# Kernel tuning notes

Hardware: AMD Instinct MI355X
Metric: run time of the kernel (lower is better)

Reference implementation:

```python
import jax, jax.numpy as jnp
import numpy as np

B, T, N, D = 2, 256, 128, 512
H = 8
D_INNER, D_STATE, D_CONV, DT_RANK = 2 * D, 16, 4, D // 16  # mamba defaults
EPS = 1e-5


def setup_inputs() -> dict:
    key = jax.random.key(0)
    ks = iter(jax.random.split(key, 32))
    g = lambda shape, s=0.02: jax.random.normal(next(ks), shape, dtype=jnp.float32) * s
    return {
        "x": jax.random.normal(next(ks), (B, T, N, D), dtype=jnp.float32),
        "mha_in_w": g((3 * D, D)), "mha_in_b": jnp.zeros((3 * D,), jnp.float32),
        "mha_out_w": g((D, D)), "mha_out_b": jnp.zeros((D,), jnp.float32),
        "n1_w": jnp.ones((D,), jnp.float32),
        "n2_w": jnp.ones((D,), jnp.float32),
        "n3_w": jnp.ones((D,), jnp.float32),
        "m_in_w": g((2 * D_INNER, D)),
        "m_conv_w": g((D_INNER, 1, D_CONV), 0.1), "m_conv_b": jnp.zeros((D_INNER,), jnp.float32),
        "m_xproj_w": g((DT_RANK + 2 * D_STATE, D_INNER)),
        "m_dt_w": g((D_INNER, DT_RANK)), "m_dt_b": jnp.full((D_INNER,), -4.6, jnp.float32),
        "m_A_log": jnp.tile(jnp.log(jnp.arange(1, D_STATE + 1, dtype=jnp.float32)), (D_INNER, 1)),
        "m_D": jnp.ones((D_INNER,), jnp.float32),
        "m_out_w": g((D, D_INNER)),
        "mlp_w1": g((2 * D, D)), "mlp_b1": jnp.zeros((2 * D,), jnp.float32),
        "mlp_w2": g((D, 2 * D)), "mlp_b2": jnp.zeros((D,), jnp.float32),
    }


def rmsnorm(x, w):
    return x * jax.lax.rsqrt(jnp.mean(x * x, axis=-1, keepdims=True) + EPS) * w


def mha(x, in_w, in_b, out_w, out_b):
    # x: (Bt, N, D); torch nn.MultiheadAttention with batch_first=True
    Bt, n, d = x.shape
    dh = d // H
    qkv = x @ in_w.T + in_b
    q, k, v = jnp.split(qkv, 3, axis=-1)
    q = q.reshape(Bt, n, H, dh)
    k = k.reshape(Bt, n, H, dh)
    v = v.reshape(Bt, n, H, dh)
    att = jax.nn.softmax(jnp.einsum('bnhd,bmhd->bhnm', q, k) / jnp.sqrt(jnp.float32(dh)), axis=-1)
    o = jnp.einsum('bhnm,bmhd->bnhd', att, v).reshape(Bt, n, d)
    return o @ out_w.T + out_b


def mamba(x, in_w, conv_w, conv_b, xproj_w, dt_w, dt_b, A_log, Dp, out_w):
    # x: (Bm, L, D)  -- standard mamba_ssm Mamba block (expand=2, d_state=16, d_conv=4)
    Bm, L, _ = x.shape
    xz = x @ in_w.T                      # (Bm, L, 2*d_inner)
    xm, z = jnp.split(xz, 2, axis=-1)
    # causal depthwise conv1d along time
    xc = jnp.pad(xm.transpose(0, 2, 1), ((0, 0), (0, 0), (D_CONV - 1, 0)))
    xc = jax.lax.conv_general_dilated(xc, conv_w, (1,), 'VALID',
                                      dimension_numbers=('NCH', 'OIH', 'NCH'),
                                      feature_group_count=D_INNER)
    xm = jax.nn.silu(xc.transpose(0, 2, 1) + conv_b)   # (Bm, L, d_inner)
    x_dbl = xm @ xproj_w.T
    dt, Bs, Cs = jnp.split(x_dbl, [DT_RANK, DT_RANK + D_STATE], axis=-1)
    dt = jax.nn.softplus(dt @ dt_w.T + dt_b)           # (Bm, L, d_inner)
    A = -jnp.exp(A_log)                                # (d_inner, d_state)

    def step(h, inp):
        dt_t, B_t, C_t, u_t = inp                      # (Bm,d_in),(Bm,ds),(Bm,ds),(Bm,d_in)
        dA = jnp.exp(dt_t[:, :, None] * A)             # (Bm, d_inner, d_state)
        h = dA * h + (dt_t * u_t)[:, :, None] * B_t[:, None, :]
        y = jnp.einsum('bds,bs->bd', h, C_t)
        return h, y

    h0 = jnp.zeros((Bm, D_INNER, D_STATE), x.dtype)
    inputs = (dt.transpose(1, 0, 2), Bs.transpose(1, 0, 2),
              Cs.transpose(1, 0, 2), xm.transpose(1, 0, 2))
    _, ys = jax.lax.scan(step, h0, inputs)
    y = ys.transpose(1, 0, 2) + xm * Dp
    y = y * jax.nn.silu(z)
    return y @ out_w.T


def reference(x, mha_in_w, mha_in_b, mha_out_w, mha_out_b, n1_w, n2_w, n3_w,
              m_in_w, m_conv_w, m_conv_b, m_xproj_w, m_dt_w, m_dt_b, m_A_log, m_D, m_out_w,
              mlp_w1, mlp_b1, mlp_w2, mlp_b2):
    Bx, Tx, Nx, Dx = x.shape
    # spatial attention over regions
    xs = x.reshape(Bx * Tx, Nx, Dx)
    xs = rmsnorm(xs + mha(xs, mha_in_w, mha_in_b, mha_out_w, mha_out_b), n1_w)
    # temporal mamba over time
    xt = xs.reshape(Bx, Tx, Nx, Dx).transpose(0, 2, 1, 3).reshape(Bx * Nx, Tx, Dx)
    xt = rmsnorm(xt + mamba(xt, m_in_w, m_conv_w, m_conv_b, m_xproj_w,
                            m_dt_w, m_dt_b, m_A_log, m_D, m_out_w), n2_w)
    # MLP (1 hidden layer, width 2*D, ReLU)
    x3 = xt.reshape(Bx, Nx, Tx, Dx).transpose(0, 2, 1, 3)
    h = jax.nn.relu(x3 @ mlp_w1.T + mlp_b1) @ mlp_w2.T + mlp_b2
    return rmsnorm(x3 + h, n3_w)
```

## Files before the change

### kernel.cpp

```cpp
#include <hip/hip_runtime.h>

typedef unsigned short u16;
typedef unsigned int u32;
typedef __attribute__((ext_vector_type(8))) short short8;
typedef __attribute__((ext_vector_type(4))) float f32x4;

__device__ __forceinline__ float bf2f(u16 u){ union{u32 i; float f;} v; v.i=((u32)u)<<16; return v.f; }
__device__ __forceinline__ u16 f2bf(float f){ union{float f; u32 i;} v; v.f=f; u32 r=v.i+0x7FFFu+((v.i>>16)&1u); return (u16)(r>>16); }

__device__ __forceinline__ void glds16(const u16* g, u16* lds){
  __builtin_amdgcn_global_load_lds((const __attribute__((address_space(1))) u32*)g,
                                   (__attribute__((address_space(3))) u32*)lds, 16, 0, 0);
}

__global__ __launch_bounds__(256) void cvt_kernel(const float* __restrict__ src, u16* __restrict__ dst, int n4){
  int i = blockIdx.x*256 + threadIdx.x;
  if (i >= n4) return;
  float4 v = ((const float4*)src)[i];
  union { u16 o[4]; uint2 q; } t;
  t.o[0]=f2bf(v.x); t.o[1]=f2bf(v.y); t.o[2]=f2bf(v.z); t.o[3]=f2bf(v.w);
  ((uint2*)dst)[i] = t.q;
}

template<int BM, int BN, int EPI>
__global__ __launch_bounds__(256, 2) void gemm_bt_kernel(
    const u16* __restrict__ A, int lda,
    const u16* __restrict__ B,
    const float* __restrict__ bias,
    u16* __restrict__ C, int ldc,
    int N, int K)
{
  constexpr int RM = BM/32, RN = BN/32;
  constexpr int AI = BM/64, BI = BN/64;
  const int tid = threadIdx.x;
  const int wave = tid>>6, lane = tid&63;
  const int wm = wave>>1, wn = wave&1;
  const int lm = lane&15, quad = lane>>4;
  const int bm0 = blockIdx.x*BM, bn0 = blockIdx.y*BN;
  __shared__ __align__(16) u16 As[BM*32];
  __shared__ __align__(16) u16 Bs[BN*32];
  f32x4 acc[RM][RN] = {};
  const int vr = tid>>2, vc = (tid&3)<<3;
  for (int k0=0; k0<K; k0+=32){
    __syncthreads();
    #pragma unroll
    for (int i=0;i<AI;i++)
      glds16(A + (size_t)(bm0 + i*64 + vr)*lda + k0 + vc, &As[(i*256 + wave*64)*8]);
    #pragma unroll
    for (int i=0;i<BI;i++)
      glds16(B + (size_t)(bn0 + i*64 + vr)*K + k0 + vc, &Bs[(i*256 + wave*64)*8]);
    __syncthreads();
    short8 af[RM], bfr[RN];
    #pragma unroll
    for (int i=0;i<RM;i++) af[i] = *(const short8*)(&As[(wm*(BM/2)+i*16+lm)*32 + quad*8]);
    #pragma unroll
    for (int j=0;j<RN;j++) bfr[j] = *(const short8*)(&Bs[(wn*(BN/2)+j*16+lm)*32 + quad*8]);
    #pragma unroll
    for (int i=0;i<RM;i++)
      #pragma unroll
      for (int j=0;j<RN;j++)
        acc[i][j] = __builtin_amdgcn_mfma_f32_16x16x32_bf16(af[i], bfr[j], acc[i][j], 0,0,0);
  }
  #pragma unroll
  for (int j=0;j<RN;j++){
    int col = bn0 + wn*(BN/2) + j*16 + lm;
    float bv = 0.f;
    if (EPI >= 1) bv = bias[col];
    #pragma unroll
    for (int i=0;i<RM;i++){
      int r0 = bm0 + wm*(BM/2) + i*16 + quad*4;
      #pragma unroll
      for (int r=0;r<4;r++){
        float v = acc[i][j][r] + bv;
        if (EPI == 2) v = fmaxf(v, 0.f);
        if (EPI == 3) v = (v > 20.f) ? v : log1pf(__expf(v));
        C[(size_t)(r0+r)*ldc + col] = f2bf(v);
      }
    }
  }
}

__global__ __launch_bounds__(256, 2) void attn_kernel(const u16* __restrict__ qkv, u16* __restrict__ o)
{
  const int bb = blockIdx.x >> 3;
  const int hh = blockIdx.x & 7;
  const int tid = threadIdx.x;
  const int wave = tid>>6, lane = tid&63;
  const int lm = lane&15, quad = lane>>4;
  __shared__ union {
    struct { u16 Q[128][72]; u16 K[128][72]; } qk;
    u16 P[128][136];
  } sm;
  __shared__ __align__(16) u16 Vt[64][136];
  const size_t base = (size_t)bb*128*1536 + (size_t)hh*64;
  #pragma unroll
  for (int i=0;i<4;i++){
    int v = i*256 + tid;
    int r = v>>3, c = (v&7)<<3;
    *(uint4*)(&sm.qk.Q[r][c]) = *(const uint4*)(qkv + base + (size_t)r*1536 + c);
    *(uint4*)(&sm.qk.K[r][c]) = *(const uint4*)(qkv + base + 512 + (size_t)r*1536 + c);
    union { uint4 q; u16 u[8]; } vv;
    vv.q = *(const uint4*)(qkv + base + 1024 + (size_t)r*1536 + c);
    #pragma unroll
    for (int j=0;j<8;j++) Vt[c+j][r] = vv.u[j];
  }
  __syncthreads();
  f32x4 sa[2][8] = {};
  #pragma unroll
  for (int k0=0;k0<64;k0+=32){
    short8 af[2], bfr[8];
    #pragma unroll
    for (int i=0;i<2;i++) af[i] = *(const short8*)(&sm.qk.Q[wave*32+i*16+lm][k0+quad*8]);
    #pragma unroll
    for (int j=0;j<8;j++) bfr[j] = *(const short8*)(&sm.qk.K[j*16+lm][k0+quad*8]);
    #pragma unroll
    for (int i=0;i<2;i++)
      #pragma unroll
      for (int j=0;j<8;j++)
        sa[i][j] = __builtin_amdgcn_mfma_f32_16x16x32_bf16(af[i], bfr[j], sa[i][j], 0,0,0);
  }
  __syncthreads();
  #pragma unroll
  for (int i=0;i<2;i++){
    #pragma unroll
    for (int r=0;r<4;r++){
      float mx = -1e30f;
      #pragma unroll
      for (int j=0;j<8;j++) mx = fmaxf(mx, sa[i][j][r]);
      #pragma unroll
      for (int off=1; off<16; off<<=1) mx = fmaxf(mx, __shfl_xor(mx, off, 64));
      float pv[8]; float sum = 0.f;
      #pragma unroll
      for (int j=0;j<8;j++){ pv[j] = __expf((sa[i][j][r]-mx)*0.125f); sum += pv[j]; }
      #pragma unroll
      for (int off=1; off<16; off<<=1) sum += __shfl_xor(sum, off, 64);
      float inv = 1.f/sum;
      int row = wave*32 + i*16 + quad*4 + r;
      #pragma unroll
      for (int j=0;j<8;j++) sm.P[row][j*16+lm] = f2bf(pv[j]*inv);
    }
  }
  f32x4 oa[2][4] = {};
  #pragma unroll
  for (int k0=0;k0<128;k0+=32){
    short8 af[2], bfr[4];
    #pragma unroll
    for (int i=0;i<2;i++) af[i] = *(const short8*)(&sm.P[wave*32+i*16+lm][k0+quad*8]);
    #pragma unroll
    for (int j=0;j<4;j++) bfr[j] = *(const short8*)(&Vt[j*16+lm][k0+quad*8]);
    #pragma unroll
    for (int i=0;i<2;i++)
      #pragma unroll
      for (int j=0;j<4;j++)
        oa[i][j] = __builtin_amdgcn_mfma_f32_16x16x32_bf16(af[i], bfr[j], oa[i][j], 0,0,0);
  }
  #pragma unroll
  for (int i=0;i<2;i++)
    #pragma unroll
    for (int j=0;j<4;j++){
      int col = hh*64 + j*16 + lm;
      int r0 = wave*32 + i*16 + quad*4;
      #pragma unroll
      for (int r=0;r<4;r++)
        o[(size_t)(bb*128 + r0 + r)*512 + col] = f2bf(oa[i][j][r]);
    }
}

__global__ __launch_bounds__(256) void conv_silu_kernel(const u16* __restrict__ xc,
    const float* __restrict__ cw, const float* __restrict__ cb, u16* __restrict__ xm)
{
  int id = blockIdx.x*256 + threadIdx.x;
  int r = id >> 7, c8 = (id & 127) << 3;
  int t = r & 255;
  union { uint4 q; u16 u[8]; } rv[4];
  #pragma unroll
  for (int tap=0;tap<4;tap++){
    int ts = t - 3 + tap;
    if (ts >= 0) rv[tap].q = *(const uint4*)(xc + (size_t)(r-3+tap)*1024 + c8);
    else rv[tap].q = make_uint4(0,0,0,0);
  }
  union { uint4 q; u16 u[8]; } out;
  #pragma unroll
  for (int j=0;j<8;j++){
    float4 wj = ((const float4*)cw)[c8+j];
    float a = cb[c8+j];
    a += bf2f(rv[0].u[j])*wj.x + bf2f(rv[1].u[j])*wj.y + bf2f(rv[2].u[j])*wj.z + bf2f(rv[3].u[j])*wj.w;
    a = a / (1.f + __expf(-a));
    out.u[j] = f2bf(a);
  }
  *(uint4*)(xm + (size_t)r*1024 + c8) = out.q;
}

__global__ __launch_bounds__(256) void scan_kernel(
    const u16* dtp, const u16* __restrict__ xm, const u16* __restrict__ xdbl,
    const u16* __restrict__ zp, const float* __restrict__ A_log, const float* __restrict__ Dp,
    u16* yp)
{
  int bm = blockIdx.x;
  int d = blockIdx.y*256 + threadIdx.x;
  float A[16], h[16];
  #pragma unroll
  for (int s=0;s<16;s++){ A[s] = -__expf(A_log[d*16+s]); h[s] = 0.f; }
  float Dv = Dp[d];
  size_t rowbase = (size_t)bm*256;
  for (int t=0;t<256;t++){
    size_t row = rowbase + t;
    float dt = bf2f(dtp[row*1024 + d]);
    float u  = bf2f(xm[row*1024 + d]);
    union { uint4 q; u16 u[8]; } b0,b1,c0,c1;
    const u16* bc = xdbl + row*64;
    b0.q = *(const uint4*)(bc+32); b1.q = *(const uint4*)(bc+40);
    c0.q = *(const uint4*)(bc+48); c1.q = *(const uint4*)(bc+56);
    float du = dt*u, yv = 0.f;
    #pragma unroll
    for (int s=0;s<8;s++){
      h[s] = __expf(dt*A[s])*h[s] + du*bf2f(b0.u[s]);
      yv += h[s]*bf2f(c0.u[s]);
    }
    #pragma unroll
    for (int s=0;s<8;s++){
      h[8+s] = __expf(dt*A[8+s])*h[8+s] + du*bf2f(b1.u[s]);
      yv += h[8+s]*bf2f(c1.u[s]);
    }
    float z = bf2f(zp[row*1024 + d]);
    float o = (yv + u*Dv) * (z / (1.f + __expf(-z)));
    yp[row*1024 + d] = f2bf(o);
  }
}

template<int MODE>
__global__ __launch_bounds__(256) void transpose_kernel(const u16* __restrict__ in, u16* __restrict__ out){
  int id = blockIdx.x*256 + threadIdx.x;
  int row_out = id >> 6, v = (id & 63) << 3;
  int b = row_out >> 15, rem = row_out & 32767;
  int row_in;
  if (MODE == 0){ int n = rem >> 8, t = rem & 255; row_in = (b*256 + t)*128 + n; }
  else          { int t = rem >> 7, n = rem & 127; row_in = (b*128 + n)*256 + t; }
  *(uint4*)(out + (size_t)row_out*512 + v) = *(const uint4*)(in + (size_t)row_in*512 + v);
}

template<bool RES_F32, bool OUT_F32>
__global__ __launch_bounds__(256) void rmsnorm_kernel(const u16* mn,
    const void* res, const float* __restrict__ w, void* out)
{
  int row = blockIdx.x*4 + (threadIdx.x>>6);
  int lane = threadIdx.x & 63;
  size_t base = (size_t)row*512 + lane*8;
  union { uint4 q; u16 u[8]; } mv;
  mv.q = *(const uint4*)(mn + base);
  float vals[8];
  if (RES_F32){
    const float* rp = (const float*)res + base;
    float4 r0 = ((const float4*)rp)[0];
    float4 r1 = ((const float4*)rp)[1];
    float rr[8] = {r0.x,r0.y,r0.z,r0.w,r1.x,r1.y,r1.z,r1.w};
    #pragma unroll
    for (int j=0;j<8;j++) vals[j] = bf2f(mv.u[j]) + rr[j];
  } else {
    union { uint4 q; u16 u[8]; } rv;
    rv.q = *(const uint4*)((const u16*)res + base);
    #pragma unroll
    for (int j=0;j<8;j++) vals[j] = bf2f(mv.u[j]) + bf2f(rv.u[j]);
  }
  float ss = 0.f;
  #pragma unroll
  for (int j=0;j<8;j++) ss += vals[j]*vals[j];
  #pragma unroll
  for (int off=1; off<64; off<<=1) ss += __shfl_xor(ss, off, 64);
  float sc = rsqrtf(ss*(1.f/512.f) + 1e-5f);
  if (OUT_F32){
    float* op = (float*)out + base;
    float o[8];
    #pragma unroll
    for (int j=0;j<8;j++) o[j] = vals[j]*sc*w[lane*8+j];
    ((float4*)op)[0] = make_float4(o[0],o[1],o[2],o[3]);
    ((float4*)op)[1] = make_float4(o[4],o[5],o[6],o[7]);
  } else {
    union { uint4 q; u16 u[8]; } ov;
    #pragma unroll
    for (int j=0;j<8;j++) ov.u[j] = f2bf(vals[j]*sc*w[lane*8+j]);
    *(uint4*)((u16*)out + base) = ov.q;
  }
}

static size_t req_bytes(int NC){
  size_t R = 65536/NC;
  size_t regB = (R*2048 > 33554432ull) ? R*2048 : 33554432ull;
  return 2ull * (4194304ull + 33554432ull + regB + R*2560ull);
}

extern "C" void kernel_launch(void* const* d_in, const int* in_sizes, int n_in,
                              void* d_out, int out_size, void* d_ws, size_t ws_size,
                              hipStream_t stream)
{
  const float* x       = (const float*)d_in[0];
  const float* w_qkv_f = (const float*)d_in[1];
  const float* b_qkv   = (const float*)d_in[2];
  const float* w_out_f = (const float*)d_in[3];
  const float* b_out   = (const float*)d_in[4];
  const float* n1w     = (const float*)d_in[5];
  const float* n2w     = (const float*)d_in[6];
  const float* n3w     = (const float*)d_in[7];
  const float* w_min_f = (const float*)d_in[8];
  const float* convw   = (const float*)d_in[9];
  const float* convb   = (const float*)d_in[10];
  const float* w_xp_f  = (const float*)d_in[11];
  const float* w_dt_f  = (const float*)d_in[12];
  const float* b_dt    = (const float*)d_in[13];
  const float* A_log   = (const float*)d_in[14];
  const float* Dp      = (const float*)d_in[15];
  const float* w_mo_f  = (const float*)d_in[16];
  const float* w_1_f   = (const float*)d_in[17];
  const float* b_1     = (const float*)d_in[18];
  const float* w_2_f   = (const float*)d_in[19];
  const float* b_2     = (const float*)d_in[20];
  float* out = (float*)d_out;
  u16* wsu = (u16*)d_ws;

  int NC = 16;
  if      (ws_size >= req_bytes(1)) NC = 1;
  else if (ws_size >= req_bytes(2)) NC = 2;
  else if (ws_size >= req_bytes(4)) NC = 4;
  else if (ws_size >= req_bytes(8)) NC = 8;
  const size_t R = 65536/NC;

  u16* w_qkv = wsu;
  u16* w_o   = w_qkv + 786432;
  u16* w_mi  = w_o   + 262144;
  u16* w_xp  = w_mi  + 1048576;
  u16* w_dt  = w_xp  + 65536;
  u16* w_mo  = w_dt  + 32768;
  u16* w_1   = w_mo  + 524288;
  u16* w_2   = w_1   + 524288;
  u16* xt    = wsu + 4194304;
  const size_t baseB = 37748736;
  const size_t regB  = (R*2048 > 33554432ull) ? R*2048 : 33554432ull;
  const size_t baseC = baseB + regB;
  u16* o2    = wsu + baseB;
  u16* x3    = wsu + baseB;
  u16* zb    = wsu + baseB;
  u16* xmb   = wsu + baseB + R*1024;
  u16* xbf_c = wsu + baseC;
  u16* qkv_c = wsu + baseC + R*512;
  u16* oat_c = wsu + baseC + R*2048;
  u16* slab  = wsu + baseC;
  u16* xdbl_c= wsu + baseC + R*1024;
  u16* mo_c  = wsu + baseC + R*1088;
  u16* h1_c  = wsu + baseC;
  u16* h2_c  = wsu + baseC + R*1024;

  struct CV { const float* s; u16* d; int n; };
  const CV cvs[] = {
    {w_qkv_f, w_qkv, 786432}, {w_out_f, w_o, 262144}, {w_min_f, w_mi, 1048576},
    {w_xp_f, w_xp, 65536}, {w_dt_f, w_dt, 32768}, {w_mo_f, w_mo, 524288},
    {w_1_f, w_1, 524288}, {w_2_f, w_2, 524288},
  };
  for (int i = 0; i < 8; i++){
    int n4 = cvs[i].n / 4;
    cvt_kernel<<<(n4+255)/256, 256, 0, stream>>>(cvs[i].s, cvs[i].d, n4);
  }

  for (int c = 0; c < NC; c++){
    cvt_kernel<<<R/2, 256, 0, stream>>>(x + c*R*512, xbf_c, (int)(R*128));
    gemm_bt_kernel<128,128,1><<<dim3(R/128,12), 256, 0, stream>>>(xbf_c, 512, w_qkv, b_qkv, qkv_c, 1536, 1536, 512);
    attn_kernel<<<(R/128)*8, 256, 0, stream>>>(qkv_c, oat_c);
    gemm_bt_kernel<128,128,1><<<dim3(R/128,4), 256, 0, stream>>>(oat_c, 512, w_o, b_out, o2 + c*R*512, 512, 512, 512);
  }
  rmsnorm_kernel<true,false><<<16384, 256, 0, stream>>>(o2, x, n1w, o2);
  transpose_kernel<0><<<16384, 256, 0, stream>>>(o2, xt);

  for (int c = 0; c < NC; c++){
    const u16* xtc = xt + c*R*512;
    gemm_bt_kernel<128,128,0><<<dim3(R/128,8), 256, 0, stream>>>(xtc, 512, w_mi, nullptr, slab, 1024, 1024, 512);
    gemm_bt_kernel<128,128,0><<<dim3(R/128,8), 256, 0, stream>>>(xtc, 512, w_mi + 524288, nullptr, zb, 1024, 1024, 512);
    conv_silu_kernel<<<R/2, 256, 0, stream>>>(slab, convw, convb, xmb);
    gemm_bt_kernel<128,64,0><<<dim3(R/128,1), 256, 0, stream>>>(xmb, 1024, w_xp, nullptr, xdbl_c, 64, 64, 1024);
    gemm_bt_kernel<128,128,3><<<dim3(R/128,8), 256, 0, stream>>>(xdbl_c, 64, w_dt, b_dt, slab, 1024, 1024, 32);
    scan_kernel<<<dim3(R/256,4), 256, 0, stream>>>(slab, xmb, xdbl_c, zb, A_log, Dp, slab);
    gemm_bt_kernel<128,128,0><<<dim3(R/128,4), 256, 0, stream>>>(slab, 1024, w_mo, nullptr, mo_c, 512, 512, 1024);
    rmsnorm_kernel<false,false><<<R/4, 256, 0, stream>>>(mo_c, xtc, n2w, (void*)xtc);
  }
  transpose_kernel<1><<<16384, 256, 0, stream>>>(xt, x3);

  for (int c = 0; c < NC; c++){
    const u16* x3c = x3 + c*R*512;
    gemm_bt_kernel<128,128,2><<<dim3(R/128,8), 256, 0, stream>>>(x3c, 512, w_1, b_1, h1_c, 1024, 1024, 512);
    gemm_bt_kernel<128,128,1><<<dim3(R/128,4), 256, 0, stream>>>(h1_c, 1024, w_2, b_2, h2_c, 512, 512, 1024);
    rmsnorm_kernel<false,true><<<R/4, 256, 0, stream>>>(h2_c, x3c, n3w, out + c*R*512);
  }
}
```

Baseline: 1.971 ms.

## Split scan state across thread pairs, prefetch next step, use exp powers

The selective scan now gives each channel two threads that each hold 8 of the 16 states, combining partial outputs with a lane shuffle, and the grid doubles to match. Inputs for step t+1 are loaded during step t to hide memory latency. When A equals -(s+1) (checked at runtime, with a general fallback), the per-state exponentials are replaced by powers of a single exp(-dt). This cuts serial latency per thread and transcendental work, at the cost of a shuffle per step, half the threads idling on stores, and a data-dependent branch.

```diff
diff --git a/kernel.cpp b/kernel.cpp
--- a/kernel.cpp
+++ b/kernel.cpp
@@ -191,40 +191,67 @@
   *(uint4*)(xm + (size_t)r*1024 + c8) = out.q;
 }
 
+typedef union { uint4 q; u16 u[8]; } BC8;
 __global__ __launch_bounds__(256) void scan_kernel(
     const u16* dtp, const u16* __restrict__ xm, const u16* __restrict__ xdbl,
     const u16* __restrict__ zp, const float* __restrict__ A_log, const float* __restrict__ Dp,
     u16* yp)
 {
-  int bm = blockIdx.x;
-  int d = blockIdx.y*256 + threadIdx.x;
-  float A[16], h[16];
-  #pragma unroll
-  for (int s=0;s<16;s++){ A[s] = -__expf(A_log[d*16+s]); h[s] = 0.f; }
-  float Dv = Dp[d];
-  size_t rowbase = (size_t)bm*256;
+  const int bm = blockIdx.x;
+  const int half = threadIdx.x & 1;
+  const int d = blockIdx.y*128 + (threadIdx.x >> 1);
+  const int s0 = half*8;
+  float A[8], h[8];
+  bool fast = true;
+  #pragma unroll
+  for (int s=0;s<8;s++){
+    A[s] = -__expf(A_log[d*16 + s0 + s]);
+    float tgt = (float)(s0 + s + 1);
+    fast = fast && (fabsf(A[s] + tgt) <= 1e-4f*tgt);
+    h[s] = 0.f;
+  }
+  const float Dv = Dp[d];
+  const size_t rowbase = (size_t)bm*256;
+  float dt = bf2f(dtp[rowbase*1024 + d]);
+  float u  = bf2f(xm[rowbase*1024 + d]);
+  BC8 bv, cv;
+  bv.q = *(const uint4*)(xdbl + rowbase*64 + 32 + s0);
+  cv.q = *(const uint4*)(xdbl + rowbase*64 + 48 + s0);
   for (int t=0;t<256;t++){
-    size_t row = rowbase + t;
-    float dt = bf2f(dtp[row*1024 + d]);
-    float u  = bf2f(xm[row*1024 + d]);
-    union { uint4 q; u16 u[8]; } b0,b1,c0,c1;
-    const u16* bc = xdbl + row*64;
-    b0.q = *(const uint4*)(bc+32); b1.q = *(const uint4*)(bc+40);
-    c0.q = *(const uint4*)(bc+48); c1.q = *(const uint4*)(bc+56);
-    float du = dt*u, yv = 0.f;
-    #pragma unroll
-    for (int s=0;s<8;s++){
-      h[s] = __expf(dt*A[s])*h[s] + du*bf2f(b0.u[s]);
-      yv += h[s]*bf2f(c0.u[s]);
+    const size_t rown = rowbase + ((t+1) & 255);
+    float dtn = bf2f(dtp[rown*1024 + d]);
+    float un  = bf2f(xm[rown*1024 + d]);
+    BC8 bn, cn;
+    bn.q = *(const uint4*)(xdbl + rown*64 + 32 + s0);
+    cn.q = *(const uint4*)(xdbl + rown*64 + 48 + s0);
+    const float du = dt*u;
+    float yv = 0.f;
+    if (fast){
+      const float e1 = __expf(-dt);
+      const float e2=e1*e1, e3=e2*e1, e4=e2*e2;
+      const float e5=e4*e1, e6=e4*e2, e7=e4*e3, e8=e4*e4;
+      const float pw[8] = {e1,e2,e3,e4,e5,e6,e7,e8};
+      const float sc = half ? e8 : 1.f;
+      #pragma unroll
+      for (int s=0;s<8;s++){
+        h[s] = (pw[s]*sc)*h[s] + du*bf2f(bv.u[s]);
+        yv += h[s]*bf2f(cv.u[s]);
+      }
+    } else {
+      #pragma unroll
+      for (int s=0;s<8;s++){
+        h[s] = __expf(dt*A[s])*h[s] + du*bf2f(bv.u[s]);
+        yv += h[s]*bf2f(cv.u[s]);
+      }
     }
-    #pragma unroll
-    for (int s=0;s<8;s++){
-      h[8+s] = __expf(dt*A[8+s])*h[8+s] + du*bf2f(b1.u[s]);
-      yv += h[8+s]*bf2f(c1.u[s]);
+    const float yo = __shfl_xor(yv, 1, 64);
+    if (!half){
+      const size_t row = rowbase + t;
+      float z = bf2f(zp[row*1024 + d]);
+      float o = (yv + yo + u*Dv) * (z / (1.f + __expf(-z)));
+      yp[row*1024 + d] = f2bf(o);
     }
-    float z = bf2f(zp[row*1024 + d]);
-    float o = (yv + u*Dv) * (z / (1.f + __expf(-z)));
-    yp[row*1024 + d] = f2bf(o);
+    dt = dtn; u = un; bv = bn; cv = cn;
   }
 }
 
@@ -376,7 +403,7 @@
     conv_silu_kernel<<<R/2, 256, 0, stream>>>(slab, convw, convb, xmb);
     gemm_bt_kernel<128,64,0><<<dim3(R/128,1), 256, 0, stream>>>(xmb, 1024, w_xp, nullptr, xdbl_c, 64, 64, 1024);
     gemm_bt_kernel<128,128,3><<<dim3(R/128,8), 256, 0, stream>>>(xdbl_c, 64, w_dt, b_dt, slab, 1024, 1024, 32);
-    scan_kernel<<<dim3(R/256,4), 256, 0, stream>>>(slab, xmb, xdbl_c, zb, A_log, Dp, slab);
+    scan_kernel<<<dim3(R/256,8), 256, 0, stream>>>(slab, xmb, xdbl_c, zb, A_log, Dp, slab);
     gemm_bt_kernel<128,128,0><<<dim3(R/128,4), 256, 0, stream>>>(slab, 1024, w_mo, nullptr, mo_c, 512, 512, 1024);
     rmsnorm_kernel<false,false><<<R/4, 256, 0, stream>>>(mo_c, xtc, n2w, (void*)xtc);
   }
```

Result: slower. 2.148 ms (+9.0%).
